# Performance work log

Measured on AMD Instinct MI355X. Metric: run time of the kernel, lower is better.

## Reference

```python
import jax, jax.numpy as jnp
import numpy as np

B, N, IN_DIM, HID, HEADS, K = 2, 2048, 1024, 512, 8, 8
HD = HID // HEADS
EPS = 1e-5
SCALE = float(1.0 / np.sqrt(HD))

def _ln(x, g, b):
    m = jnp.mean(x, -1, keepdims=True)
    v = jnp.var(x, -1, keepdims=True)
    return (x - m) * jax.lax.rsqrt(v + EPS) * g + b

def setup_inputs() -> dict:
    key = jax.random.key(0)
    ks = jax.random.split(key, 40)
    def p(k, shape):
        return jax.random.normal(k, shape, jnp.float32) * 0.02
    z = lambda *s: jnp.zeros(s, jnp.float32)
    o = lambda *s: jnp.ones(s, jnp.float32)
    return {
        "x": jax.random.normal(ks[0], (B, N, IN_DIM), jnp.float32),
        # fc_start: Linear(in,hid) + GLU Linear(hid,2*hid)
        "w_start": p(ks[1], (HID, IN_DIM)), "b_start": z(HID),
        "glu_w": p(ks[2], (2 * HID, HID)), "glu_b": z(2 * HID),
        # 2 GCN layers (stacked on leading axis)
        "gcn_w": p(ks[3], (2, HID, HID)), "gcn_b": z(2, HID),
        "gcn_g": o(2, HID), "gcn_beta": z(2, HID),
        # 2 transformer layers
        "qkv_w": p(ks[4], (2, 3 * HID, HID)), "qkv_b": z(2, 3 * HID),
        "out_w": p(ks[5], (2, HID, HID)), "out_b": z(2, HID),
        "ln1_g": o(2, HID), "ln1_b": z(2, HID),
        "ffn_w1": p(ks[6], (2, 2 * HID, HID)), "ffn_b1": z(2, 2 * HID),
        "ffn_w2": p(ks[7], (2, HID, 2 * HID)), "ffn_b2": z(2, HID),
        "ln2_g": o(2, HID), "ln2_b": z(2, HID),
        # fusion, attention pooling, classifier
        "fus_w": p(ks[8], (HID, 2 * HID)), "fus_b": z(HID),
        "attn_w1": p(ks[9], (256, HID)), "attn_b1": z(256),
        "attn_w2": p(ks[10], (1, 256)), "attn_b2": z(1),
        "cls_w1": p(ks[11], (HID // 2, HID)), "cls_b1": z(HID // 2),
        "cls_w2": p(ks[12], (1, HID // 2)), "cls_b2": z(1),
    }

def reference(x, w_start, b_start, glu_w, glu_b, gcn_w, gcn_b, gcn_g, gcn_beta,
              qkv_w, qkv_b, out_w, out_b, ln1_g, ln1_b, ffn_w1, ffn_b1,
              ffn_w2, ffn_b2, ln2_g, ln2_b, fus_w, fus_b,
              attn_w1, attn_b1, attn_w2, attn_b2,
              cls_w1, cls_b1, cls_w2, cls_b2):
    # fc_start: Linear -> GLU (dropout off in eval)
    h = x @ w_start.T + b_start
    vg = h @ glu_w.T + glu_b
    val, gate = jnp.split(vg, 2, -1)
    h = val * jax.nn.sigmoid(gate)                      # [B,N,HID]

    # dynamic KNN graph: cdist + topk + scatter + sym-normalize
    sq = jnp.sum(h * h, -1)
    d2 = sq[:, :, None] + sq[:, None, :] - 2.0 * jnp.einsum('bnc,bmc->bnm', h, h)
    dist = jnp.sqrt(jnp.maximum(d2, 0.0))
    _, idx = jax.lax.top_k(-dist, K + 1)                # nearest K+1 (incl self)
    bi = jnp.arange(B)[:, None, None]
    ri = jnp.arange(N)[None, :, None]
    adj = jnp.zeros((B, N, N), h.dtype).at[bi, ri, idx].set(1.0)
    rs = jnp.sum(adj, -1)
    dinv = jnp.where(rs > 0, rs ** -0.5, 0.0)
    adj = adj * dinv[:, :, None] * dinv[:, None, :]     # == D^-1/2 A D^-1/2

    # GCN branch
    hg = h
    for i in range(2):
        s = hg @ gcn_w[i].T + gcn_b[i]
        o = jnp.einsum('bnm,bmc->bnc', adj, s)
        o = _ln(o, gcn_g[i], gcn_beta[i])
        hg = jax.nn.leaky_relu(o, 0.2) + hg

    # Transformer branch (post-LN)
    ht = h
    for i in range(2):
        qkv = ht @ qkv_w[i].T + qkv_b[i]
        q, k_, v = jnp.split(qkv, 3, -1)
        q = q.reshape(B, N, HEADS, HD)
        k_ = k_.reshape(B, N, HEADS, HD)
        v = v.reshape(B, N, HEADS, HD)
        att = jax.nn.softmax(jnp.einsum('bqhd,bkhd->bhqk', q, k_) * SCALE, -1)
        ao = jnp.einsum('bhqk,bkhd->bqhd', att, v).reshape(B, N, HID)
        ao = ao @ out_w[i].T + out_b[i]
        ht = _ln(ht + ao, ln1_g[i], ln1_b[i])
        ff = jax.nn.gelu(ht @ ffn_w1[i].T + ffn_b1[i], approximate=False) @ ffn_w2[i].T + ffn_b2[i]
        ht = _ln(ht + ff, ln2_g[i], ln2_b[i])

    hf = jnp.concatenate([hg, ht], -1) @ fus_w.T + fus_b  # [B,N,HID]

    # gated attention pooling
    a = jnp.tanh(hf @ attn_w1.T + attn_b1) @ attn_w2.T + attn_b2
    a = jax.nn.softmax(a, axis=1)                       # [B,N,1]
    M = jnp.sum(hf * a, axis=1)                         # [B,HID]

    logits = jax.nn.elu(M @ cls_w1.T + cls_b1) @ cls_w2.T + cls_b2  # [B,1]
    return logits, a, M
```

## Files before the change

kernel.cpp:

```cpp
#include <hip/hip_runtime.h>
#include <hip/hip_bf16.h>
#include <math.h>

#define NSEQ 2048
#define ROWS 4096
#define KNN 9
#define MB (1ull << 20)

typedef short bh8 __attribute__((ext_vector_type(8)));
typedef float f4v __attribute__((ext_vector_type(4)));
typedef unsigned long long u64k;

__device__ __forceinline__ short f2bf(float f) {
    union { float f; unsigned u; } v; v.f = f;
    unsigned r = (v.u + 0x7fffu + ((v.u >> 16) & 1u)) >> 16;
    return (short)r;
}
__device__ __forceinline__ float b2f(short s) {
    union { unsigned u; float f; } v; v.u = ((unsigned)(unsigned short)s) << 16; return v.f;
}

__device__ __forceinline__ void gload16(const void* g, void* l) {
    __builtin_amdgcn_global_load_lds(
        (const __attribute__((address_space(1))) void*)g,
        (__attribute__((address_space(3))) void*)l, 16, 0, 0);
}

__device__ __forceinline__ float blockReduceSum(float v, float* red) {
    int tid = threadIdx.x;
    red[tid] = v; __syncthreads();
    for (int s = 128; s > 0; s >>= 1) {
        if (tid < s) red[tid] += red[tid + s];
        __syncthreads();
    }
    float r = red[0]; __syncthreads();
    return r;
}

struct CvtArgs { const float* src[10]; short* dst[10]; int n4[10]; };
__global__ __launch_bounds__(256) void cvt_k(CvtArgs a) {
    int s = blockIdx.y;
    const float* sp = a.src[s]; short* dp = a.dst[s]; int n = a.n4[s];
    for (int i = blockIdx.x * 256 + threadIdx.x; i < n; i += gridDim.x * 256) {
        float4 v = ((const float4*)sp)[i];
        short4 o; o.x = f2bf(v.x); o.y = f2bf(v.y); o.z = f2bf(v.z); o.w = f2bf(v.w);
        ((short4*)dp)[i] = o;
    }
}

template <int OUTMODE>
__device__ __forceinline__ void gemm_epilogue(int row, int col, int N, const f4v& a,
        float bv, float* Cf, short* Cb, short* Kb_, short* Vt_)
{
    if (OUTMODE == 3) {
        int b = row >> 11, n0 = row & 2047;
        if (col < 512) {
            int h = col >> 6, d = col & 63;
            size_t base = (((size_t)(b * 8 + h) * NSEQ + n0) << 6) + d;
            #pragma unroll
            for (int rr = 0; rr < 4; ++rr)
                Cb[base + ((size_t)rr << 6)] = f2bf((a[rr] + bv) * 0.18033688f);
        } else if (col < 1024) {
            int cc = col - 512, h = cc >> 6, d = cc & 63;
            size_t base = (((size_t)(b * 8 + h) * NSEQ + n0) << 6) + d;
            #pragma unroll
            for (int rr = 0; rr < 4; ++rr)
                Kb_[base + ((size_t)rr << 6)] = f2bf(a[rr] + bv);
        } else {
            int cc = col - 1024, h = cc >> 6, d = cc & 63;
            short4 ov;
            ov.x = f2bf(a[0] + bv); ov.y = f2bf(a[1] + bv);
            ov.z = f2bf(a[2] + bv); ov.w = f2bf(a[3] + bv);
            *(short4*)(Vt_ + (((size_t)((b * 8 + h) * 64 + d)) << 11) + n0) = ov;
        }
    } else {
        #pragma unroll
        for (int rr = 0; rr < 4; ++rr) {
            float v = a[rr] + bv;
            if (OUTMODE == 0) Cf[(size_t)(row + rr) * N + col] = v;
            else if (OUTMODE == 1) Cb[(size_t)(row + rr) * N + col] = f2bf(v);
            else if (OUTMODE == 2) {
                Cf[(size_t)(row + rr) * N + col] = v;
                Cb[(size_t)(row + rr) * N + col] = f2bf(v);
            } else if (OUTMODE == 4) {
                Cb[(size_t)(row + rr) * N + col] = f2bf(0.5f * v * (1.f + erff(v * 0.70710678118654752f)));
            } else if (OUTMODE == 5) {
                Cf[(size_t)(row + rr) * N + col] = tanhf(v);
            }
        }
    }
}

template <int OUTMODE>
__global__ __launch_bounds__(256) void mfma_gemm(
        const short* __restrict__ A, const short* __restrict__ W,
        const float* __restrict__ bias, float* __restrict__ Cf, short* __restrict__ Cb,
        int M, int N, int K)
{
    __shared__ short As[2][64 * 64];
    __shared__ short Bs[2][64 * 64];
    int tid = threadIdx.x;
    int wv = tid >> 6, l = tid & 63;
    int g = l >> 4, c = l & 15;
    int wr = wv >> 1, wc = wv & 1;
    int bm = blockIdx.y * 64, bn = blockIdx.x * 64;
    int sr = l >> 3, sc = ((l & 7) ^ sr) * 8;
    const short* Ap = A + (size_t)(bm + wv * 16 + sr) * K + sc;
    const short* Wp = W + (size_t)(bn + wv * 16 + sr) * K + sc;
    int ldsB = (wv * 16) * 64;

    #define GSTAGE(buf, k0) { \
        gload16(Ap + (k0), &As[buf][ldsB]); \
        gload16(Ap + (size_t)8 * K + (k0), &As[buf][ldsB + 8 * 64]); \
        gload16(Wp + (k0), &Bs[buf][ldsB]); \
        gload16(Wp + (size_t)8 * K + (k0), &Bs[buf][ldsB + 8 * 64]); }

    f4v acc[2][2] = {};
    GSTAGE(0, 0);
    __syncthreads();
    int nk = K >> 6;
    for (int t = 0; t < nk; ++t) {
        int cur = t & 1;
        if (t + 1 < nk) GSTAGE(cur ^ 1, (t + 1) << 6);
        #pragma unroll
        for (int ks = 0; ks < 2; ++ks) {
            bh8 af[2], bf_[2];
            #pragma unroll
            for (int mi = 0; mi < 2; ++mi) {
                int row = wr * 32 + mi * 16 + c;
                af[mi] = *(const bh8*)(&As[cur][row * 64 + (((ks * 4 + g) ^ (c & 7)) * 8)]);
            }
            #pragma unroll
            for (int ni = 0; ni < 2; ++ni) {
                int row = wc * 32 + ni * 16 + c;
                bf_[ni] = *(const bh8*)(&Bs[cur][row * 64 + (((ks * 4 + g) ^ (c & 7)) * 8)]);
            }
            #pragma unroll
            for (int mi = 0; mi < 2; ++mi)
                #pragma unroll
                for (int ni = 0; ni < 2; ++ni)
                    acc[mi][ni] = __builtin_amdgcn_mfma_f32_16x16x32_bf16(af[mi], bf_[ni], acc[mi][ni], 0, 0, 0);
        }
        __syncthreads();
    }
    #undef GSTAGE
    short* Kb_ = (OUTMODE == 3) ? Cb + 2097152 : nullptr;
    short* Vt_ = (OUTMODE == 3) ? Cb + 4194304 : nullptr;
    #pragma unroll
    for (int mi = 0; mi < 2; ++mi) {
        int row = bm + wr * 32 + mi * 16 + g * 4;
        #pragma unroll
        for (int ni = 0; ni < 2; ++ni) {
            int col = bn + wc * 32 + ni * 16 + c;
            gemm_epilogue<OUTMODE>(row, col, N, acc[mi][ni], bias[col], Cf, Cb, Kb_, Vt_);
        }
    }
}

__global__ __launch_bounds__(256) void mfma_gram(
        const short* __restrict__ Hi0, const short* __restrict__ Lo0,
        const float* __restrict__ SQ0, float* __restrict__ D2a, float* __restrict__ D2b)
{
    __shared__ short HiR[64 * 64], LoR[64 * 64], HiC[64 * 64], LoC[64 * 64];
    int tid = threadIdx.x;
    int bz = blockIdx.z;
    const short* Hi = Hi0 + (size_t)bz * NSEQ * 512;
    const short* Lo = Lo0 + (size_t)bz * NSEQ * 512;
    const float* SQ = SQ0 + bz * NSEQ;
    float* D2 = bz ? D2b : D2a;
    int wv = tid >> 6, l = tid & 63;
    int g = l >> 4, c = l & 15;
    int wr = wv >> 1, wc = wv & 1;
    int bm = blockIdx.y * 64, bn = blockIdx.x * 64;
    int sr = l >> 3, sc = ((l & 7) ^ sr) * 8;
    const short* hiR = Hi + (size_t)(bm + wv * 16 + sr) * 512 + sc;
    const short* loR = Lo + (size_t)(bm + wv * 16 + sr) * 512 + sc;
    const short* hiC = Hi + (size_t)(bn + wv * 16 + sr) * 512 + sc;
    const short* loC = Lo + (size_t)(bn + wv * 16 + sr) * 512 + sc;
    int ldsOff = (wv * 16) * 64;
    f4v acc[2][2] = {};
    for (int k0 = 0; k0 < 512; k0 += 64) {
        __syncthreads();
        gload16(hiR + k0, HiR + ldsOff);
        gload16(hiR + (size_t)8 * 512 + k0, HiR + ldsOff + 8 * 64);
        gload16(loR + k0, LoR + ldsOff);
        gload16(loR + (size_t)8 * 512 + k0, LoR + ldsOff + 8 * 64);
        gload16(hiC + k0, HiC + ldsOff);
        gload16(hiC + (size_t)8 * 512 + k0, HiC + ldsOff + 8 * 64);
        gload16(loC + k0, LoC + ldsOff);
        gload16(loC + (size_t)8 * 512 + k0, LoC + ldsOff + 8 * 64);
        __syncthreads();
        #pragma unroll
        for (int ks = 0; ks < 2; ++ks) {
            bh8 hr[2], lr_[2], hc[2], lc[2];
            #pragma unroll
            for (int mi = 0; mi < 2; ++mi) {
                int o = (wr * 32 + mi * 16 + c) * 64 + (((ks * 4 + g) ^ (c & 7)) * 8);
                hr[mi] = *(const bh8*)(HiR + o);
                lr_[mi] = *(const bh8*)(LoR + o);
            }
            #pragma unroll
            for (int ni = 0; ni < 2; ++ni) {
                int o = (wc * 32 + ni * 16 + c) * 64 + (((ks * 4 + g) ^ (c & 7)) * 8);
                hc[ni] = *(const bh8*)(HiC + o);
                lc[ni] = *(const bh8*)(LoC + o);
            }
            #pragma unroll
            for (int mi = 0; mi < 2; ++mi)
                #pragma unroll
                for (int ni = 0; ni < 2; ++ni) {
                    acc[mi][ni] = __builtin_amdgcn_mfma_f32_16x16x32_bf16(hr[mi], hc[ni], acc[mi][ni], 0, 0, 0);
                    acc[mi][ni] = __builtin_amdgcn_mfma_f32_16x16x32_bf16(hr[mi], lc[ni], acc[mi][ni], 0, 0, 0);
                    acc[mi][ni] = __builtin_amdgcn_mfma_f32_16x16x32_bf16(lr_[mi], hc[ni], acc[mi][ni], 0, 0, 0);
                }
        }
    }
    #pragma unroll
    for (int mi = 0; mi < 2; ++mi) {
        int row = bm + wr * 32 + mi * 16 + g * 4;
        #pragma unroll
        for (int ni = 0; ni < 2; ++ni) {
            int col = bn + wc * 32 + ni * 16 + c;
            float sqc = SQ[col];
            #pragma unroll
            for (int rr = 0; rr < 4; ++rr)
                D2[(size_t)(row + rr) * NSEQ + col] = SQ[row + rr] + sqc - 2.f * acc[mi][ni][rr];
        }
    }
}

__global__ __launch_bounds__(256) void topk9_k(const float* __restrict__ D2a,
                                               const float* __restrict__ D2b, int* __restrict__ idx)
{
    int ng = blockIdx.x, tid = threadIdx.x;
    const float* D2 = (ng >> 11) ? D2b : D2a;
    int n = ng & 2047;
    __shared__ u64k lists[256][9];
    u64k a[8];
    union { float f; unsigned u; } cv;
    #pragma unroll
    for (int j = 0; j < 8; ++j) {
        int mcol = tid + j * 256;
        cv.f = fmaxf(D2[(size_t)n * NSEQ + mcol], 0.f);
        a[j] = ((u64k)cv.u << 32) | (unsigned)mcol;
    }
    #define CE(i,j) { u64k x = a[i], y = a[j]; bool t = x < y; a[i] = t ? x : y; a[j] = t ? y : x; }
    CE(0,1) CE(2,3) CE(4,5) CE(6,7)
    CE(0,2) CE(1,3) CE(4,6) CE(5,7)
    CE(1,2) CE(5,6)
    CE(0,4) CE(1,5) CE(2,6) CE(3,7)
    CE(2,4) CE(3,5)
    CE(1,2) CE(3,4) CE(5,6)
    #undef CE
    #pragma unroll
    for (int j = 0; j < 8; ++j) lists[tid][j] = a[j];
    lists[tid][8] = ~0ull;
    __syncthreads();
    for (int s = 128; s >= 1; s >>= 1) {
        if (tid < s) {
            u64k out[9];
            u64k* Al = lists[tid];
            u64k* Bl = lists[tid + s];
            int ia = 0, ib = 0;
            #pragma unroll
            for (int o = 0; o < 9; ++o) {
                u64k av = Al[ia], bv = Bl[ib];
                bool t = av <= bv;
                out[o] = t ? av : bv;
                ia += t; ib += !t;
            }
            #pragma unroll
            for (int o = 0; o < 9; ++o) Al[o] = out[o];
        }
        __syncthreads();
    }
    if (tid < 9) idx[ng * KNN + tid] = (int)(lists[0][tid] & 0xffffffffu);
}

__global__ __launch_bounds__(256) void gcn_post(
        const float* __restrict__ s, const int* __restrict__ idx,
        const float* __restrict__ g, const float* __restrict__ be,
        float* __restrict__ hg, short* __restrict__ hgb)
{
    int row = blockIdx.x, tid = threadIdx.x;
    int bb = row >> 11;
    __shared__ float os[512];
    __shared__ float red[256];
    int id[KNN];
    #pragma unroll
    for (int j = 0; j < KNN; ++j) id[j] = idx[row * KNN + j] + (bb << 11);
    for (int c = tid; c < 512; c += 256) {
        float acc = 0.f;
        #pragma unroll
        for (int j = 0; j < KNN; ++j) acc += s[((size_t)id[j] << 9) + c];
        os[c] = acc * (1.f / 9.f);
    }
    __syncthreads();
    float mean = blockReduceSum(os[tid] + os[tid + 256], red) * (1.f / 512.f);
    float d0 = os[tid] - mean, d1 = os[tid + 256] - mean;
    float var = blockReduceSum(d0 * d0 + d1 * d1, red) * (1.f / 512.f);
    float rs = rsqrtf(var + 1e-5f);
    size_t base = (size_t)row << 9;
    for (int c = tid; c < 512; c += 256) {
        float y = (os[c] - mean) * rs * g[c] + be[c];
        y = y > 0.f ? y : 0.2f * y;
        float nv = y + hg[base + c];
        hg[base + c] = nv;
        hgb[base + c] = f2bf(nv);
    }
}

__global__ __launch_bounds__(256) void ln_res(
        float* __restrict__ x, const float* __restrict__ r,
        const float* __restrict__ g, const float* __restrict__ b, short* __restrict__ xb)
{
    int row = blockIdx.x, tid = threadIdx.x;
    __shared__ float xs[512];
    __shared__ float red[256];
    size_t base = (size_t)row << 9;
    for (int c = tid; c < 512; c += 256) xs[c] = x[base + c] + r[base + c];
    __syncthreads();
    float mean = blockReduceSum(xs[tid] + xs[tid + 256], red) * (1.f / 512.f);
    float d0 = xs[tid] - mean, d1 = xs[tid + 256] - mean;
    float var = blockReduceSum(d0 * d0 + d1 * d1, red) * (1.f / 512.f);
    float rs = rsqrtf(var + 1e-5f);
    for (int c = tid; c < 512; c += 256) {
        float y = (xs[c] - mean) * rs * g[c] + b[c];
        x[base + c] = y;
        xb[base + c] = f2bf(y);
    }
}

__global__ __launch_bounds__(256) void flash_attn(
        const short* __restrict__ Qb, const short* __restrict__ Kb,
        const short* __restrict__ Vt, short* __restrict__ Opb, float* __restrict__ Ml)
{
    __shared__ short Ks[2][4096];
    __shared__ short Vs[2][4096];
    int tid = threadIdx.x;
    int wid = tid >> 6, lane = tid & 63;
    int g = lane >> 4, c = lane & 15;
    int s = blockIdx.y, bh = blockIdx.z;
    int q0 = blockIdx.x * 64 + wid * 16;
    int srow = lane >> 3;
    int sc8 = ((lane & 7) ^ srow) * 8;
    int w8 = wid * 8;

    const short* KbB = Kb + ((size_t)bh * NSEQ + s * 512) * 64;
    const short* VtB = Vt + (size_t)bh * 64 * NSEQ + s * 512;

    const short* qbase = Qb + ((size_t)bh * NSEQ + q0 + c) * 64 + g * 8;
    bh8 qa0 = *(const bh8*)(qbase);
    bh8 qa1 = *(const bh8*)(qbase + 32);

    f4v o0 = {0,0,0,0}, o1 = {0,0,0,0}, o2 = {0,0,0,0}, o3 = {0,0,0,0};
    float lloc = 0.f;
    float mrun = -INFINITY;
    int hi2 = g >> 1;
    int s1 = c + (((g << 1) & 3) << 4);
    int s2 = c + ((((g << 1) + 1) & 3) << 4);

    #define FSTAGE(buf, kt) { \
        const short* kp_ = KbB + (size_t)(kt) * 64 * 64; \
        gload16(kp_ + (size_t)(w8 + srow) * 64 + sc8,        &Ks[buf][w8 * 64]); \
        gload16(kp_ + (size_t)(32 + w8 + srow) * 64 + sc8,   &Ks[buf][(32 + w8) * 64]); \
        const short* vp_ = VtB + (size_t)(kt) * 64; \
        gload16(vp_ + (size_t)(w8 + srow) * NSEQ + sc8,      &Vs[buf][w8 * 64]); \
        gload16(vp_ + (size_t)(32 + w8 + srow) * NSEQ + sc8, &Vs[buf][(32 + w8) * 64]); }

    FSTAGE(0, 0);
    __syncthreads();
    for (int t = 0; t < 8; ++t) {
        int cur = t & 1;
        if (t < 7) FSTAGE(cur ^ 1, t + 1);
        f4v sv[4];
        #pragma unroll
        for (int cb = 0; cb < 4; ++cb) {
            int row = cb * 16 + c;
            const short* kr = &Ks[cur][row * 64];
            bh8 kb0 = *(const bh8*)(kr + ((g ^ (row & 7)) * 8));
            bh8 kb1 = *(const bh8*)(kr + (((4 + g) ^ (row & 7)) * 8));
            f4v a = {0,0,0,0};
            a = __builtin_amdgcn_mfma_f32_16x16x32_bf16(kb0, qa0, a, 0, 0, 0);
            a = __builtin_amdgcn_mfma_f32_16x16x32_bf16(kb1, qa1, a, 0, 0, 0);
            sv[cb] = a;
        }
        float mt = fmaxf(fmaxf(fmaxf(sv[0][0], sv[0][1]), fmaxf(sv[0][2], sv[0][3])),
                         fmaxf(fmaxf(sv[1][0], sv[1][1]), fmaxf(sv[1][2], sv[1][3])));
        mt = fmaxf(mt, fmaxf(fmaxf(sv[2][0], sv[2][1]), fmaxf(sv[2][2], sv[2][3])));
        mt = fmaxf(mt, fmaxf(fmaxf(sv[3][0], sv[3][1]), fmaxf(sv[3][2], sv[3][3])));
        mt = fmaxf(mt, __shfl_xor(mt, 16));
        mt = fmaxf(mt, __shfl_xor(mt, 32));
        if (__any(mt > mrun + 6.f)) {
            float mn = fmaxf(mrun, mt);
            float al = __builtin_amdgcn_exp2f(mrun - mn);
            mrun = mn;
            o0 *= al; o1 *= al; o2 *= al; o3 *= al; lloc *= al;
        }
        unsigned wv_[8];
        #pragma unroll
        for (int cb = 0; cb < 4; ++cb) {
            float p0 = __builtin_amdgcn_exp2f(sv[cb][0] - mrun);
            float p1 = __builtin_amdgcn_exp2f(sv[cb][1] - mrun);
            float p2 = __builtin_amdgcn_exp2f(sv[cb][2] - mrun);
            float p3 = __builtin_amdgcn_exp2f(sv[cb][3] - mrun);
            lloc += (p0 + p1) + (p2 + p3);
            asm("v_cvt_pk_bf16_f32 %0, %1, %2" : "=v"(wv_[cb * 2])     : "v"(p0), "v"(p1));
            asm("v_cvt_pk_bf16_f32 %0, %1, %2" : "=v"(wv_[cb * 2 + 1]) : "v"(p2), "v"(p3));
        }
        union { unsigned u[4]; bh8 h; } pa0u, pa1u;
        {
            unsigned t0 = __shfl((int)wv_[0], s1), t2 = __shfl((int)wv_[2], s1);
            unsigned t1 = __shfl((int)wv_[1], s1), t3 = __shfl((int)wv_[3], s1);
            unsigned u0 = __shfl((int)wv_[0], s2), u2 = __shfl((int)wv_[2], s2);
            unsigned u1 = __shfl((int)wv_[1], s2), u3 = __shfl((int)wv_[3], s2);
            pa0u.u[0] = hi2 ? t2 : t0;
            pa0u.u[1] = hi2 ? t3 : t1;
            pa0u.u[2] = hi2 ? u2 : u0;
            pa0u.u[3] = hi2 ? u3 : u1;
        }
        {
            unsigned t0 = __shfl((int)wv_[4], s1), t2 = __shfl((int)wv_[6], s1);
            unsigned t1 = __shfl((int)wv_[5], s1), t3 = __shfl((int)wv_[7], s1);
            unsigned u0 = __shfl((int)wv_[4], s2), u2 = __shfl((int)wv_[6], s2);
            unsigned u1 = __shfl((int)wv_[5], s2), u3 = __shfl((int)wv_[7], s2);
            pa1u.u[0] = hi2 ? t2 : t0;
            pa1u.u[1] = hi2 ? t3 : t1;
            pa1u.u[2] = hi2 ? u2 : u0;
            pa1u.u[3] = hi2 ? u3 : u1;
        }
        #pragma unroll
        for (int db = 0; db < 4; ++db) {
            int row = db * 16 + c;
            const short* vr = &Vs[cur][row * 64];
            bh8 vb0 = *(const bh8*)(vr + ((g ^ (row & 7)) * 8));
            bh8 vb1 = *(const bh8*)(vr + (((4 + g) ^ (row & 7)) * 8));
            f4v* op = (db == 0) ? &o0 : (db == 1) ? &o1 : (db == 2) ? &o2 : &o3;
            *op = __builtin_amdgcn_mfma_f32_16x16x32_bf16(vb0, pa0u.h, *op, 0, 0, 0);
            *op = __builtin_amdgcn_mfma_f32_16x16x32_bf16(vb1, pa1u.h, *op, 0, 0, 0);
        }
        __syncthreads();
    }
    #undef FSTAGE
    float lsum = lloc;
    lsum += __shfl_xor(lsum, 16);
    lsum += __shfl_xor(lsum, 32);
    size_t qrow = ((size_t)(s * 16 + bh) * NSEQ) + q0 + c;
    size_t rb = qrow * 64 + g * 4;
    #pragma unroll
    for (int r = 0; r < 4; ++r) {
        Opb[rb + r]      = f2bf(o0[r]);
        Opb[rb + 16 + r] = f2bf(o1[r]);
        Opb[rb + 32 + r] = f2bf(o2[r]);
        Opb[rb + 48 + r] = f2bf(o3[r]);
    }
    if (g == 0) {
        Ml[qrow * 2]     = mrun;
        Ml[qrow * 2 + 1] = lsum;
    }
}

__global__ __launch_bounds__(256) void merge_k(const short* __restrict__ Opb, const float* __restrict__ Ml,
                                               short* __restrict__ aob)
{
    int idx = blockIdx.x * 256 + threadIdx.x;
    int d = idx & 63, q = (idx >> 6) & 2047, bh = idx >> 17;
    float M = -INFINITY;
    float mv[4], lv[4];
    #pragma unroll
    for (int s = 0; s < 4; ++s) {
        size_t r = (size_t)(s * 16 + bh) * NSEQ + q;
        mv[s] = Ml[r * 2]; lv[s] = Ml[r * 2 + 1];
        M = fmaxf(M, mv[s]);
    }
    float L = 0.f, num = 0.f;
    #pragma unroll
    for (int s = 0; s < 4; ++s) {
        float w = __builtin_amdgcn_exp2f(mv[s] - M);
        L += lv[s] * w;
        num += b2f(Opb[((size_t)(s * 16 + bh) * NSEQ + q) * 64 + d]) * w;
    }
    int b = bh >> 3, h = bh & 7;
    aob[((size_t)(b * NSEQ + q)) * 512 + h * 64 + d] = f2bf(num / L);
}

__global__ __launch_bounds__(256) void glu_row_k(const float* __restrict__ vg, float* __restrict__ h,
        float* __restrict__ hgf, short* __restrict__ hi, short* __restrict__ lo,
        float* __restrict__ sq) {
    int row = blockIdx.x, tid = threadIdx.x;
    __shared__ float red[256];
    size_t vb = (size_t)row << 10;
    size_t hb = (size_t)row << 9;
    float ss = 0.f;
    #pragma unroll
    for (int j = 0; j < 2; ++j) {
        int c = tid + j * 256;
        float v = vg[vb + c], gt = vg[vb + 512 + c];
        float hv = v * (1.f / (1.f + __expf(-gt)));
        h[hb + c] = hv; hgf[hb + c] = hv;
        short hbb = f2bf(hv);
        hi[hb + c] = hbb;
        lo[hb + c] = f2bf(hv - b2f(hbb));
        ss = fmaf(hv, hv, ss);
    }
    float sm = blockReduceSum(ss, red);
    if (tid == 0) sq[row] = sm;
}

__global__ void concat_bf(const short* __restrict__ hgb, const short* __restrict__ htb,
                          short* __restrict__ cat) {
    for (int i = blockIdx.x * 256 + threadIdx.x; i < ROWS * 256; i += gridDim.x * 256) {
        int row = i >> 8, c4 = (i & 255) * 4;
        short4 v = (c4 < 512) ? *(const short4*)(hgb + ((size_t)row << 9) + c4)
                              : *(const short4*)(htb + ((size_t)row << 9) + c4 - 512);
        *(short4*)(cat + ((size_t)row << 10) + c4) = v;
    }
}

__global__ __launch_bounds__(256) void rowdot_k(const float* __restrict__ t, const float* __restrict__ w2,
                                                const float* __restrict__ b2, float* __restrict__ srow) {
    int row = blockIdx.x, tid = threadIdx.x;
    __shared__ float red[256];
    float s = blockReduceSum(t[(size_t)row * 256 + tid] * w2[tid], red);
    if (tid == 0) srow[row] = s + b2[0];
}
__global__ __launch_bounds__(256) void softmax_n_k(const float* __restrict__ srow, float* __restrict__ a,
                                                   float* __restrict__ out) {
    int b = blockIdx.x, tid = threadIdx.x;
    __shared__ float red[256];
    float mx = -INFINITY;
    for (int n = tid; n < NSEQ; n += 256) mx = fmaxf(mx, srow[b * NSEQ + n]);
    red[tid] = mx; __syncthreads();
    for (int s = 128; s > 0; s >>= 1) {
        if (tid < s) red[tid] = fmaxf(red[tid], red[tid + s]);
        __syncthreads();
    }
    mx = red[0]; __syncthreads();
    float sm = 0.f;
    for (int n = tid; n < NSEQ; n += 256) {
        float e = expf(srow[b * NSEQ + n] - mx);
        a[b * NSEQ + n] = e; sm += e;
    }
    float inv = 1.f / blockReduceSum(sm, red);
    for (int n = tid; n < NSEQ; n += 256) {
        float v = a[b * NSEQ + n] * inv;
        a[b * NSEQ + n] = v;
        out[2 + b * NSEQ + n] = v;
    }
}
__global__ __launch_bounds__(256) void pool_part(const float* __restrict__ hf, const float* __restrict__ a,
                                                 float* __restrict__ part) {
    int b = blockIdx.y, chunk = blockIdx.x, tid = threadIdx.x;
    float a0 = 0.f, a1 = 0.f;
    for (int r = 0; r < 64; ++r) {
        int n = chunk * 64 + r;
        float wgt = a[b * NSEQ + n];
        const float* row = hf + ((size_t)(b * NSEQ + n) << 9);
        a0 = fmaf(row[tid], wgt, a0);
        a1 = fmaf(row[tid + 256], wgt, a1);
    }
    part[((b * 32 + chunk) << 9) + tid] = a0;
    part[((b * 32 + chunk) << 9) + tid + 256] = a1;
}
__global__ __launch_bounds__(256) void pool_fin(const float* __restrict__ part, float* __restrict__ Mb,
                                                float* __restrict__ out) {
    int b = blockIdx.x, tid = threadIdx.x;
    float s0 = 0.f, s1 = 0.f;
    for (int ch = 0; ch < 32; ++ch) {
        s0 += part[((b * 32 + ch) << 9) + tid];
        s1 += part[((b * 32 + ch) << 9) + tid + 256];
    }
    Mb[b * 512 + tid] = s0; Mb[b * 512 + tid + 256] = s1;
    out[2 + ROWS + b * 512 + tid] = s0; out[2 + ROWS + b * 512 + tid + 256] = s1;
}
__global__ __launch_bounds__(256) void classifier_k(const float* __restrict__ Mb,
        const float* __restrict__ w1, const float* __restrict__ b1,
        const float* __restrict__ w2, const float* __restrict__ b2, float* __restrict__ out) {
    int b = blockIdx.x, tid = threadIdx.x;
    __shared__ float Ms[512];
    __shared__ float red[256];
    for (int c = tid; c < 512; c += 256) Ms[c] = Mb[b * 512 + c];
    __syncthreads();
    float acc = 0.f;
    for (int c = 0; c < 512; ++c) acc = fmaf(Ms[c], w1[tid * 512 + c], acc);
    acc += b1[tid];
    float hj = acc > 0.f ? acc : expm1f(acc);
    float s = blockReduceSum(hj * w2[tid], red);
    if (tid == 0) out[b] = s + b2[0];
}

extern "C" void kernel_launch(void* const* d_in, const int* in_sizes, int n_in,
                              void* d_out, int out_size, void* d_ws, size_t ws_size,
                              hipStream_t stream)
{
    const float* X      = (const float*)d_in[0];
    const float* Wstart = (const float*)d_in[1];
    const float* Bstart = (const float*)d_in[2];
    const float* GluW   = (const float*)d_in[3];
    const float* GluB   = (const float*)d_in[4];
    const float* GcnW   = (const float*)d_in[5];
    const float* GcnB   = (const float*)d_in[6];
    const float* GcnG   = (const float*)d_in[7];
    const float* GcnBe  = (const float*)d_in[8];
    const float* QkvW   = (const float*)d_in[9];
    const float* QkvB   = (const float*)d_in[10];
    const float* OutW   = (const float*)d_in[11];
    const float* OutB   = (const float*)d_in[12];
    const float* Ln1G   = (const float*)d_in[13];
    const float* Ln1B   = (const float*)d_in[14];
    const float* Ffn1W  = (const float*)d_in[15];
    const float* Ffn1B  = (const float*)d_in[16];
    const float* Ffn2W  = (const float*)d_in[17];
    const float* Ffn2B  = (const float*)d_in[18];
    const float* Ln2G   = (const float*)d_in[19];
    const float* Ln2B   = (const float*)d_in[20];
    const float* FusW   = (const float*)d_in[21];
    const float* FusB   = (const float*)d_in[22];
    const float* AW1    = (const float*)d_in[23];
    const float* AB1    = (const float*)d_in[24];
    const float* AW2    = (const float*)d_in[25];
    const float* AB2    = (const float*)d_in[26];
    const float* CW1    = (const float*)d_in[27];
    const float* CB1    = (const float*)d_in[28];
    const float* CW2    = (const float*)d_in[29];
    const float* CB2    = (const float*)d_in[30];
    float* out = (float*)d_out;

    if (ws_size < 86 * MB) return;

    char* w = (char*)d_ws;
    short* Wb = (short*)w;
    short* wbStart = Wb;
    short* wbGlu   = Wb + 524288;
    short* wbGcn   = Wb + 1048576;
    short* wbQkv   = Wb + 1572864;
    short* wbOut   = Wb + 3145728;
    short* wbFfn1  = Wb + 3670016;
    short* wbFfn2  = Wb + 4718592;
    short* wbFus   = Wb + 5767168;
    short* wbAw1   = Wb + 6291456;
    float* sq   = (float*)(w + 13 * MB);
    int*   idx  = (int*)  (w + 13 * MB + (16u << 10));
    float* srow = (float*)(w + 13 * MB + (176u << 10));
    float* afb  = (float*)(w + 13 * MB + (192u << 10));
    float* Mbuf = (float*)(w + 13 * MB + (208u << 10));
    float* part = (float*)(w + 13 * MB + (212u << 10));
    short* Xbf  = (short*)(w + 14 * MB);
    float* hg   = (float*)(w + 14 * MB);
    short* hpreb= (short*)(w + 22 * MB);
    short* hgb  = (short*)(w + 22 * MB);
    float* big  = (float*)(w + 26 * MB);
    short* Opb  = (short*)(w + 26 * MB);
    float* Ml   = (float*)(w + 42 * MB);
    float* ffn2o= (float*)(w + 42 * MB);
    float* h    = (float*)(w + 50 * MB);
    short* hhi  = (short*)(w + 58 * MB);
    short* hlo  = (short*)(w + 62 * MB);
    short* htb  = (short*)(w + 62 * MB);
    float* hf   = (float*)(w + 58 * MB);
    float* D2b1 = (float*)(w + 66 * MB);
    short* hfb  = (short*)(w + 66 * MB);
    short* aob  = (short*)(w + 70 * MB);
    float* t256 = (float*)(w + 70 * MB);
    short* Qb   = (short*)(w + 74 * MB);
    short* Kb   = (short*)(w + 78 * MB);
    short* Vt   = (short*)(w + 82 * MB);
    short* ffb  = (short*)(w + 74 * MB);
    short* catb = (short*)(w + 74 * MB);

    dim3 blk(256);

    CvtArgs ca;
    ca.src[0] = X;     ca.dst[0] = Xbf;     ca.n4[0] = ROWS * 1024 / 4;
    ca.src[1] = Wstart;ca.dst[1] = wbStart; ca.n4[1] = 524288 / 4;
    ca.src[2] = GluW;  ca.dst[2] = wbGlu;   ca.n4[2] = 524288 / 4;
    ca.src[3] = GcnW;  ca.dst[3] = wbGcn;   ca.n4[3] = 524288 / 4;
    ca.src[4] = QkvW;  ca.dst[4] = wbQkv;   ca.n4[4] = 1572864 / 4;
    ca.src[5] = OutW;  ca.dst[5] = wbOut;   ca.n4[5] = 524288 / 4;
    ca.src[6] = Ffn1W; ca.dst[6] = wbFfn1;  ca.n4[6] = 1048576 / 4;
    ca.src[7] = Ffn2W; ca.dst[7] = wbFfn2;  ca.n4[7] = 1048576 / 4;
    ca.src[8] = FusW;  ca.dst[8] = wbFus;   ca.n4[8] = 524288 / 4;
    ca.src[9] = AW1;   ca.dst[9] = wbAw1;   ca.n4[9] = 131072 / 4;
    cvt_k<<<dim3(256, 10), blk, 0, stream>>>(ca);

    mfma_gemm<1><<<dim3(8, 64), blk, 0, stream>>>(Xbf, wbStart, Bstart, nullptr, hpreb, ROWS, 512, 1024);
    mfma_gemm<0><<<dim3(16, 64), blk, 0, stream>>>(hpreb, wbGlu, GluB, big, nullptr, ROWS, 1024, 512);
    glu_row_k<<<dim3(ROWS), blk, 0, stream>>>(big, h, hg, hhi, hlo, sq);

    mfma_gram<<<dim3(32, 32, 2), blk, 0, stream>>>(hhi, hlo, sq, big, D2b1);
    topk9_k<<<dim3(ROWS), blk, 0, stream>>>(big, D2b1, idx);

    const short* gA = hhi;
    for (int i = 0; i < 2; ++i) {
        mfma_gemm<0><<<dim3(8, 64), blk, 0, stream>>>(gA, wbGcn + (size_t)i * 262144,
                                                      GcnB + i * 512, big, nullptr, ROWS, 512, 512);
        gcn_post<<<dim3(ROWS), blk, 0, stream>>>(big, idx, GcnG + i * 512, GcnBe + i * 512, hg, hgb);
        gA = hgb;
    }

    const short* tA = hhi;
    for (int i = 0; i < 2; ++i) {
        mfma_gemm<3><<<dim3(24, 64), blk, 0, stream>>>(tA, wbQkv + (size_t)i * 786432,
                                                       QkvB + i * 1536, nullptr, Qb, ROWS, 1536, 512);
        flash_attn<<<dim3(32, 4, 16), blk, 0, stream>>>(Qb, Kb, Vt, Opb, Ml);
        merge_k<<<dim3(8192), blk, 0, stream>>>(Opb, Ml, aob);
        mfma_gemm<0><<<dim3(8, 64), blk, 0, stream>>>(aob, wbOut + (size_t)i * 262144,
                                                      OutB + i * 512, big, nullptr, ROWS, 512, 512);
        ln_res<<<dim3(ROWS), blk, 0, stream>>>(h, big, Ln1G + i * 512, Ln1B + i * 512, htb);
        mfma_gemm<4><<<dim3(16, 64), blk, 0, stream>>>(htb, wbFfn1 + (size_t)i * 524288,
                                                       Ffn1B + i * 1024, nullptr, ffb, ROWS, 1024, 512);
        mfma_gemm<0><<<dim3(8, 64), blk, 0, stream>>>(ffb, wbFfn2 + (size_t)i * 524288,
                                                      Ffn2B + i * 512, ffn2o, nullptr, ROWS, 512, 1024);
        ln_res<<<dim3(ROWS), blk, 0, stream>>>(h, ffn2o, Ln2G + i * 512, Ln2B + i * 512, htb);
        tA = htb;
    }

    concat_bf<<<dim3(2048), blk, 0, stream>>>(hgb, htb, catb);
    mfma_gemm<2><<<dim3(8, 64), blk, 0, stream>>>(catb, wbFus, FusB, hf, hfb, ROWS, 512, 1024);

    mfma_gemm<5><<<dim3(4, 64), blk, 0, stream>>>(hfb, wbAw1, AB1, t256, nullptr, ROWS, 256, 512);
    rowdot_k<<<dim3(ROWS), blk, 0, stream>>>(t256, AW2, AB2, srow);
    softmax_n_k<<<dim3(2), blk, 0, stream>>>(srow, afb, out);
    pool_part<<<dim3(32, 2), blk, 0, stream>>>(hf, afb, part);
    pool_fin<<<dim3(2), blk, 0, stream>>>(part, Mbuf, out);

    classifier_k<<<dim3(2), blk, 0, stream>>>(Mbuf, CW1, CB1, CW2, CB2, out);
}
```

Before: 425.8 us.

## Fuse concat into fusion GEMM and keep residual streams in bf16

The fusion GEMM gains a CAT mode that reads its A tiles straight from the two 512-wide bf16 branch outputs, so the separate concat kernel and its buffer go away. The fp32 copies of the GLU output and the two residual streams are also dropped. GCN post-processing and the LayerNorm residual kernels now read and write bf16 tensors, in place where possible. This cuts launches and global-memory traffic, but residual additions now accumulate from bf16-rounded values, which lowers numerical precision.

```diff
diff --git a/kernel.cpp b/kernel.cpp
--- a/kernel.cpp
+++ b/kernel.cpp
@@ -91,9 +91,10 @@
     }
 }
 
-template <int OUTMODE>
+template <int OUTMODE, int CAT>
 __global__ __launch_bounds__(256) void mfma_gemm(
-        const short* __restrict__ A, const short* __restrict__ W,
+        const short* __restrict__ A, const short* __restrict__ A2,
+        const short* __restrict__ W,
         const float* __restrict__ bias, float* __restrict__ Cf, short* __restrict__ Cb,
         int M, int N, int K)
 {
@@ -105,13 +106,17 @@
     int wr = wv >> 1, wc = wv & 1;
     int bm = blockIdx.y * 64, bn = blockIdx.x * 64;
     int sr = l >> 3, sc = ((l & 7) ^ sr) * 8;
-    const short* Ap = A + (size_t)(bm + wv * 16 + sr) * K + sc;
+    int arow = bm + wv * 16 + sr;
+    size_t astr = CAT ? 512 : (size_t)K;
+    const short* Ap  = A  + (size_t)arow * astr + sc;
+    const short* Ap2 = CAT ? (A2 + (size_t)arow * 512 + sc) : nullptr;
     const short* Wp = W + (size_t)(bn + wv * 16 + sr) * K + sc;
     int ldsB = (wv * 16) * 64;
 
     #define GSTAGE(buf, k0) { \
-        gload16(Ap + (k0), &As[buf][ldsB]); \
-        gload16(Ap + (size_t)8 * K + (k0), &As[buf][ldsB + 8 * 64]); \
+        const short* ab_ = (CAT && (k0) >= 512) ? (Ap2 + (k0) - 512) : (Ap + (k0)); \
+        gload16(ab_, &As[buf][ldsB]); \
+        gload16(ab_ + 8 * astr, &As[buf][ldsB + 8 * 64]); \
         gload16(Wp + (k0), &Bs[buf][ldsB]); \
         gload16(Wp + (size_t)8 * K + (k0), &Bs[buf][ldsB + 8 * 64]); }
 
@@ -280,7 +285,7 @@
 __global__ __launch_bounds__(256) void gcn_post(
         const float* __restrict__ s, const int* __restrict__ idx,
         const float* __restrict__ g, const float* __restrict__ be,
-        float* __restrict__ hg, short* __restrict__ hgb)
+        const short* __restrict__ rin, short* __restrict__ rout)
 {
     int row = blockIdx.x, tid = threadIdx.x;
     int bb = row >> 11;
@@ -304,31 +309,26 @@
     for (int c = tid; c < 512; c += 256) {
         float y = (os[c] - mean) * rs * g[c] + be[c];
         y = y > 0.f ? y : 0.2f * y;
-        float nv = y + hg[base + c];
-        hg[base + c] = nv;
-        hgb[base + c] = f2bf(nv);
+        rout[base + c] = f2bf(y + b2f(rin[base + c]));
     }
 }
 
 __global__ __launch_bounds__(256) void ln_res(
-        float* __restrict__ x, const float* __restrict__ r,
-        const float* __restrict__ g, const float* __restrict__ b, short* __restrict__ xb)
+        const short* __restrict__ xin, const float* __restrict__ r,
+        const float* __restrict__ g, const float* __restrict__ b, short* __restrict__ xout)
 {
     int row = blockIdx.x, tid = threadIdx.x;
     __shared__ float xs[512];
     __shared__ float red[256];
     size_t base = (size_t)row << 9;
-    for (int c = tid; c < 512; c += 256) xs[c] = x[base + c] + r[base + c];
+    for (int c = tid; c < 512; c += 256) xs[c] = b2f(xin[base + c]) + r[base + c];
     __syncthreads();
     float mean = blockReduceSum(xs[tid] + xs[tid + 256], red) * (1.f / 512.f);
     float d0 = xs[tid] - mean, d1 = xs[tid + 256] - mean;
     float var = blockReduceSum(d0 * d0 + d1 * d1, red) * (1.f / 512.f);
     float rs = rsqrtf(var + 1e-5f);
-    for (int c = tid; c < 512; c += 256) {
-        float y = (xs[c] - mean) * rs * g[c] + b[c];
-        x[base + c] = y;
-        xb[base + c] = f2bf(y);
-    }
+    for (int c = tid; c < 512; c += 256)
+        xout[base + c] = f2bf((xs[c] - mean) * rs * g[c] + b[c]);
 }
 
 __global__ __launch_bounds__(256) void flash_attn(
@@ -484,9 +484,8 @@
     aob[((size_t)(b * NSEQ + q)) * 512 + h * 64 + d] = f2bf(num / L);
 }
 
-__global__ __launch_bounds__(256) void glu_row_k(const float* __restrict__ vg, float* __restrict__ h,
-        float* __restrict__ hgf, short* __restrict__ hi, short* __restrict__ lo,
-        float* __restrict__ sq) {
+__global__ __launch_bounds__(256) void glu_row_k(const float* __restrict__ vg,
+        short* __restrict__ hi, short* __restrict__ lo, float* __restrict__ sq) {
     int row = blockIdx.x, tid = threadIdx.x;
     __shared__ float red[256];
     size_t vb = (size_t)row << 10;
@@ -497,7 +496,6 @@
         int c = tid + j * 256;
         float v = vg[vb + c], gt = vg[vb + 512 + c];
         float hv = v * (1.f / (1.f + __expf(-gt)));
-        h[hb + c] = hv; hgf[hb + c] = hv;
         short hbb = f2bf(hv);
         hi[hb + c] = hbb;
         lo[hb + c] = f2bf(hv - b2f(hbb));
@@ -505,16 +503,6 @@
     }
     float sm = blockReduceSum(ss, red);
     if (tid == 0) sq[row] = sm;
-}
-
-__global__ void concat_bf(const short* __restrict__ hgb, const short* __restrict__ htb,
-                          short* __restrict__ cat) {
-    for (int i = blockIdx.x * 256 + threadIdx.x; i < ROWS * 256; i += gridDim.x * 256) {
-        int row = i >> 8, c4 = (i & 255) * 4;
-        short4 v = (c4 < 512) ? *(const short4*)(hgb + ((size_t)row << 9) + c4)
-                              : *(const short4*)(htb + ((size_t)row << 9) + c4 - 512);
-        *(short4*)(cat + ((size_t)row << 10) + c4) = v;
-    }
 }
 
 __global__ __launch_bounds__(256) void rowdot_k(const float* __restrict__ t, const float* __restrict__ w2,
@@ -646,18 +634,16 @@
     float* Mbuf = (float*)(w + 13 * MB + (208u << 10));
     float* part = (float*)(w + 13 * MB + (212u << 10));
     short* Xbf  = (short*)(w + 14 * MB);
-    float* hg   = (float*)(w + 14 * MB);
     short* hpreb= (short*)(w + 22 * MB);
     short* hgb  = (short*)(w + 22 * MB);
     float* big  = (float*)(w + 26 * MB);
     short* Opb  = (short*)(w + 26 * MB);
+    float* hf   = (float*)(w + 26 * MB);
     float* Ml   = (float*)(w + 42 * MB);
     float* ffn2o= (float*)(w + 42 * MB);
-    float* h    = (float*)(w + 50 * MB);
     short* hhi  = (short*)(w + 58 * MB);
     short* hlo  = (short*)(w + 62 * MB);
     short* htb  = (short*)(w + 62 * MB);
-    float* hf   = (float*)(w + 58 * MB);
     float* D2b1 = (float*)(w + 66 * MB);
     short* hfb  = (short*)(w + 66 * MB);
     short* aob  = (short*)(w + 70 * MB);
@@ -666,7 +652,6 @@
     short* Kb   = (short*)(w + 78 * MB);
     short* Vt   = (short*)(w + 82 * MB);
     short* ffb  = (short*)(w + 74 * MB);
-    short* catb = (short*)(w + 74 * MB);
 
     dim3 blk(256);
 
@@ -683,42 +668,42 @@
     ca.src[9] = AW1;   ca.dst[9] = wbAw1;   ca.n4[9] = 131072 / 4;
     cvt_k<<<dim3(256, 10), blk, 0, stream>>>(ca);
 
-    mfma_gemm<1><<<dim3(8, 64), blk, 0, stream>>>(Xbf, wbStart, Bstart, nullptr, hpreb, ROWS, 512, 1024);
-    mfma_gemm<0><<<dim3(16, 64), blk, 0, stream>>>(hpreb, wbGlu, GluB, big, nullptr, ROWS, 1024, 512);
-    glu_row_k<<<dim3(ROWS), blk, 0, stream>>>(big, h, hg, hhi, hlo, sq);
+    mfma_gemm<1, 0><<<dim3(8, 64), blk, 0, stream>>>(Xbf, nullptr, wbStart, Bstart, nullptr, hpreb, ROWS, 512, 1024);
+    mfma_gemm<0, 0><<<dim3(16, 64), blk, 0, stream>>>(hpreb, nullptr, wbGlu, GluB, big, nullptr, ROWS, 1024, 512);
+    glu_row_k<<<dim3(ROWS), blk, 0, stream>>>(big, hhi, hlo, sq);
 
     mfma_gram<<<dim3(32, 32, 2), blk, 0, stream>>>(hhi, hlo, sq, big, D2b1);
     topk9_k<<<dim3(ROWS), blk, 0, stream>>>(big, D2b1, idx);
 
     const short* gA = hhi;
+    const short* gR = hhi;
     for (int i = 0; i < 2; ++i) {
-        mfma_gemm<0><<<dim3(8, 64), blk, 0, stream>>>(gA, wbGcn + (size_t)i * 262144,
-                                                      GcnB + i * 512, big, nullptr, ROWS, 512, 512);
-        gcn_post<<<dim3(ROWS), blk, 0, stream>>>(big, idx, GcnG + i * 512, GcnBe + i * 512, hg, hgb);
-        gA = hgb;
+        mfma_gemm<0, 0><<<dim3(8, 64), blk, 0, stream>>>(gA, nullptr, wbGcn + (size_t)i * 262144,
+                                                         GcnB + i * 512, big, nullptr, ROWS, 512, 512);
+        gcn_post<<<dim3(ROWS), blk, 0, stream>>>(big, idx, GcnG + i * 512, GcnBe + i * 512, gR, hgb);
+        gA = hgb; gR = hgb;
     }
 
     const short* tA = hhi;
     for (int i = 0; i < 2; ++i) {
-        mfma_gemm<3><<<dim3(24, 64), blk, 0, stream>>>(tA, wbQkv + (size_t)i * 786432,
-                                                       QkvB + i * 1536, nullptr, Qb, ROWS, 1536, 512);
+        mfma_gemm<3, 0><<<dim3(24, 64), blk, 0, stream>>>(tA, nullptr, wbQkv + (size_t)i * 786432,
+                                                          QkvB + i * 1536, nullptr, Qb, ROWS, 1536, 512);
         flash_attn<<<dim3(32, 4, 16), blk, 0, stream>>>(Qb, Kb, Vt, Opb, Ml);
         merge_k<<<dim3(8192), blk, 0, stream>>>(Opb, Ml, aob);
-        mfma_gemm<0><<<dim3(8, 64), blk, 0, stream>>>(aob, wbOut + (size_t)i * 262144,
-                                                      OutB + i * 512, big, nullptr, ROWS, 512, 512);
-        ln_res<<<dim3(ROWS), blk, 0, stream>>>(h, big, Ln1G + i * 512, Ln1B + i * 512, htb);
-        mfma_gemm<4><<<dim3(16, 64), blk, 0, stream>>>(htb, wbFfn1 + (size_t)i * 524288,
-                                                       Ffn1B + i * 1024, nullptr, ffb, ROWS, 1024, 512);
-        mfma_gemm<0><<<dim3(8, 64), blk, 0, stream>>>(ffb, wbFfn2 + (size_t)i * 524288,
-                                                      Ffn2B + i * 512, ffn2o, nullptr, ROWS, 512, 1024);
-        ln_res<<<dim3(ROWS), blk, 0, stream>>>(h, ffn2o, Ln2G + i * 512, Ln2B + i * 512, htb);
+        mfma_gemm<0, 0><<<dim3(8, 64), blk, 0, stream>>>(aob, nullptr, wbOut + (size_t)i * 262144,
+                                                         OutB + i * 512, big, nullptr, ROWS, 512, 512);
+        ln_res<<<dim3(ROWS), blk, 0, stream>>>(tA, big, Ln1G + i * 512, Ln1B + i * 512, htb);
+        mfma_gemm<4, 0><<<dim3(16, 64), blk, 0, stream>>>(htb, nullptr, wbFfn1 + (size_t)i * 524288,
+                                                          Ffn1B + i * 1024, nullptr, ffb, ROWS, 1024, 512);
+        mfma_gemm<0, 0><<<dim3(8, 64), blk, 0, stream>>>(ffb, nullptr, wbFfn2 + (size_t)i * 524288,
+                                                         Ffn2B + i * 512, ffn2o, nullptr, ROWS, 512, 1024);
+        ln_res<<<dim3(ROWS), blk, 0, stream>>>(htb, ffn2o, Ln2G + i * 512, Ln2B + i * 512, htb);
         tA = htb;
     }
 
-    concat_bf<<<dim3(2048), blk, 0, stream>>>(hgb, htb, catb);
-    mfma_gemm<2><<<dim3(8, 64), blk, 0, stream>>>(catb, wbFus, FusB, hf, hfb, ROWS, 512, 1024);
-
-    mfma_gemm<5><<<dim3(4, 64), blk, 0, stream>>>(hfb, wbAw1, AB1, t256, nullptr, ROWS, 256, 512);
+    mfma_gemm<2, 1><<<dim3(8, 64), blk, 0, stream>>>(hgb, htb, wbFus, FusB, hf, hfb, ROWS, 512, 1024);
+
+    mfma_gemm<5, 0><<<dim3(4, 64), blk, 0, stream>>>(hfb, nullptr, wbAw1, AB1, t256, nullptr, ROWS, 256, 512);
     rowdot_k<<<dim3(ROWS), blk, 0, stream>>>(t256, AW2, AB2, srow);
     softmax_n_k<<<dim3(2), blk, 0, stream>>>(srow, afb, out);
     pool_part<<<dim3(32, 2), blk, 0, stream>>>(hf, afb, part);
```

Result: faster. 410.1 us (-3.7%).
